# Kernel tuning notes

Hardware: AMD Instinct MI355X
Metric: run time of the kernel (lower is better)

The kernel has to match this reference:

```python
import jax, jax.numpy as jnp
import numpy as np

N, D, F, O = 32768, 32, 128, 128  # nodes, fixed in-degree, in_feats, out_feats


def _lstm_reduce(m, W_ih, W_hh, b_ih, b_hh):
    """Run an LSTM over each node's neighbor mailbox m: [N, T, F] -> final h: [N, H].
    PyTorch gate order: i, f, g, o. W_ih: [4H, F], W_hh: [4H, H]."""
    n, _, _ = m.shape
    H = W_hh.shape[1]
    b = b_ih + b_hh

    def step(carry, x_t):
        h, c = carry
        gates = x_t @ W_ih.T + h @ W_hh.T + b  # [N, 4H]
        i, f, g, o = jnp.split(gates, 4, axis=-1)
        c = jax.nn.sigmoid(f) * c + jax.nn.sigmoid(i) * jnp.tanh(g)
        h = jax.nn.sigmoid(o) * jnp.tanh(c)
        return (h, c), None

    h0 = jnp.zeros((n, H), m.dtype)
    (h_final, _), _ = jax.lax.scan(step, (h0, h0), jnp.swapaxes(m, 0, 1))
    return h_final


def setup_inputs() -> dict:
    key = jax.random.key(0)
    ks = jax.random.split(key, 9)
    stdv_lin = 1.0 / np.sqrt(F)   # linear init: uniform(-1/sqrt(in_feats))
    stdv_lstm = 1.0 / np.sqrt(F)  # torch LSTM init: uniform(-1/sqrt(hidden))
    u = lambda k, shape, s: jax.random.uniform(k, shape, jnp.float32, -s, s)
    return {
        "feat": jax.random.normal(ks[0], (N, F), jnp.float32),
        "neigh_idx": jax.random.randint(ks[1], (N, D), 0, N, jnp.int32),
        "W_ih": u(ks[2], (4 * F, F), stdv_lstm),
        "W_hh": u(ks[3], (4 * F, F), stdv_lstm),
        "b_ih": u(ks[4], (4 * F,), stdv_lstm),
        "b_hh": u(ks[5], (4 * F,), stdv_lstm),
        "W1": u(ks[6], (O, F), stdv_lin),
        "b1": u(ks[6], (O,), stdv_lin),
        "W2": u(ks[7], (O, F), stdv_lin),
        "b2": u(ks[8], (O,), stdv_lin),
    }


def reference(feat, neigh_idx, W_ih, W_hh, b_ih, b_hh, W1, b1, W2, b2):
    # Mailbox gather: each node's D neighbor feature rows -> [N, D, F]
    m = feat[neigh_idx]
    # LSTM reducer -> final hidden state per node
    h = _lstm_reduce(m, W_ih, W_hh, b_ih, b_hh)  # [N, F]
    degs = jnp.asarray(neigh_idx.shape[1], feat.dtype)  # fixed-degree graph
    ah = h / degs
    # feat = linear1(feat) + linear2(ah)
    return feat @ W1.T + b1 + ah @ W2.T + b2
```

## Files before the change

kernel.cpp:

```cpp
#include <hip/hip_runtime.h>
#include <hip/hip_bf16.h>

#define NN 32768
#define DEG 32
#define FF 128
#define OO 128
#define MB 32
#define MB2 16

#define K1 1.4426950408889634f
#define K2 2.8853900817779268f

#define PPITCH 1040
#define P0OFF 0
#define P1OFF 16640
#define H0OFF 33280
#define H1OFF 37376
#define LDSSZ 41472

typedef __attribute__((ext_vector_type(8))) short bfrag;
typedef __attribute__((ext_vector_type(4))) float f32x4;

__device__ __forceinline__ unsigned short b16(float x) {
    unsigned u = __float_as_uint(x) + 0x8000u;
    return (unsigned short)(u >> 16);
}
__device__ __forceinline__ float bf2f(unsigned short u) {
    return __uint_as_float((unsigned)u << 16);
}
__device__ __forceinline__ bfrag pack8(float4 a, float4 b) {
    bfrag r;
    r[0] = (short)b16(a.x); r[1] = (short)b16(a.y); r[2] = (short)b16(a.z); r[3] = (short)b16(a.w);
    r[4] = (short)b16(b.x); r[5] = (short)b16(b.y); r[6] = (short)b16(b.z); r[7] = (short)b16(b.w);
    return r;
}
__device__ __forceinline__ void gload16(const void* g, void* l) {
    __builtin_amdgcn_global_load_lds(
        (const __attribute__((address_space(1))) unsigned int*)g,
        (__attribute__((address_space(3))) unsigned int*)l, 16, 0, 0);
}

__global__ void prep_weights(const float* __restrict__ wih, const float* __restrict__ whh,
                             const float* __restrict__ b_ih, const float* __restrict__ b_hh,
                             const float* __restrict__ w1, const float* __restrict__ b1,
                             const float* __restrict__ w2, const float* __restrict__ b2,
                             short* __restrict__ wihb, short* __restrict__ whhb,
                             short* __restrict__ w1b, short* __restrict__ w2b,
                             float* __restrict__ biasg, float* __restrict__ biaso)
{
    int i = blockIdx.x * blockDim.x + threadIdx.x;
    if (i < 512 * 128) { wihb[i] = (short)b16(wih[i]); whhb[i] = (short)b16(whh[i]); }
    if (i < 128 * 128) { w1b[i] = (short)b16(w1[i]); w2b[i] = (short)b16(w2[i] * 0.03125f); }
    if (i < 512) biasg[i] = b_ih[i] + b_hh[i];
    if (i < 128) biaso[i] = b1[i] + b2[i];
}

__global__ __launch_bounds__(512, 2)
void xp_gemm(const float* __restrict__ feat, const short* __restrict__ wihb,
             const float* __restrict__ biasg, unsigned short* __restrict__ xp)
{
    __shared__ short xt[MB * 128];

    const int tid  = (int)threadIdx.x;
    const int lane = tid & 63;
    const int wave = tid >> 6;
    const int n0   = (int)blockIdx.x * MB;
    const int srow = tid >> 4;
    const int cs   = tid & 15;

    {   const float4* p = reinterpret_cast<const float4*>(feat + (n0 + srow) * FF + cs * 8);
        int sb = (srow * 256 + cs * 16) ^ ((srow & 7) << 4);
        *reinterpret_cast<bfrag*>(reinterpret_cast<char*>(xt) + sb) = pack8(p[0], p[1]); }

    const int colw = wave * 16 + (lane & 15);
    bfrag wih[4][4];
#pragma unroll
    for (int g = 0; g < 4; ++g) {
        const short* pih = wihb + (g * 128 + colw) * FF + (lane >> 4) * 8;
#pragma unroll
        for (int kt = 0; kt < 4; ++kt)
            wih[g][kt] = *reinterpret_cast<const bfrag*>(pih + kt * 32);
    }
    float bg4[4];
#pragma unroll
    for (int g = 0; g < 4; ++g) bg4[g] = biasg[g * 128 + colw];

    __syncthreads();

    const int arow = lane & 15;
    const int asub = (lane >> 4) * 16;
    const int hr0  = (lane >> 4) * 4;
    const int swz  = (arow & 7) << 4;
    const char* xtp = reinterpret_cast<const char*>(xt);

#pragma unroll
    for (int rt = 0; rt < 2; ++rt) {
        bfrag a[4];
#pragma unroll
        for (int kt = 0; kt < 4; ++kt)
            a[kt] = *reinterpret_cast<const bfrag*>(xtp + (((rt * 16 + arow) * 256 + kt * 64 + asub) ^ swz));
#pragma unroll
        for (int g = 0; g < 4; ++g) {
            f32x4 acc = {bg4[g], bg4[g], bg4[g], bg4[g]};
#pragma unroll
            for (int kt = 0; kt < 4; ++kt)
                acc = __builtin_amdgcn_mfma_f32_16x16x32_bf16(a[kt], wih[g][kt], acc, 0, 0, 0);
#pragma unroll
            for (int r = 0; r < 4; ++r)
                xp[(n0 + rt * 16 + hr0 + r) * 512 + g * 128 + colw] = b16(acc[r]);
        }
    }
}

__global__ __launch_bounds__(256, 2)
void sage_xp2(const float* __restrict__ feat, const int* __restrict__ nidx,
              const unsigned short* __restrict__ xp,
              const short* __restrict__ whhb, const short* __restrict__ w1b,
              const short* __restrict__ w2b, const float* __restrict__ biaso,
              float* __restrict__ out)
{
    __shared__ char lds[LDSSZ];
    __shared__ int  idx_s[MB2 * DEG];

    const int tid  = (int)threadIdx.x;
    const int lane = tid & 63;
    const int wave = tid >> 6;
    const int n0   = (int)blockIdx.x * MB2;
    const int srow = tid >> 4;
    const int cs   = tid & 15;

    idx_s[tid]       = nidx[n0 * DEG + tid];
    idx_s[256 + tid] = nidx[n0 * DEG + 256 + tid];
    {   bfrag z = {0, 0, 0, 0, 0, 0, 0, 0};
        *reinterpret_cast<bfrag*>(lds + H0OFF + tid * 16) = z; }

    const int colb = wave * 32 + (lane & 15);
    bfrag whh[2][4][4];
#pragma unroll
    for (int ct = 0; ct < 2; ++ct)
#pragma unroll
        for (int g = 0; g < 4; ++g) {
            const short* phh = whhb + (g * 128 + colb + ct * 16) * FF + (lane >> 4) * 8;
#pragma unroll
            for (int kt = 0; kt < 4; ++kt)
                whh[ct][g][kt] = *reinterpret_cast<const bfrag*>(phh + kt * 32);
        }
    __syncthreads();

#pragma unroll
    for (int j = 0; j < 4; ++j) {
        int nd = idx_s[(wave * 4 + j) * DEG + 0];
        gload16(xp + nd * 512 + lane * 8, lds + P0OFF + (wave * 4 + j) * PPITCH);
    }
    __syncthreads();

    const int arow = lane & 15;
    const int asub = (lane >> 4) * 16;
    const int hr0  = (lane >> 4) * 4;
    const int swz  = (arow & 7) << 4;

    f32x4 cs0 = {0.f, 0.f, 0.f, 0.f};
    f32x4 cs1 = {0.f, 0.f, 0.f, 0.f};

    auto rdP = [&](const char* pc, int goff) {
        f32x4 v;
        v[0] = bf2f(*reinterpret_cast<const unsigned short*>(pc + goff));
        v[1] = bf2f(*reinterpret_cast<const unsigned short*>(pc + goff + PPITCH));
        v[2] = bf2f(*reinterpret_cast<const unsigned short*>(pc + goff + 2 * PPITCH));
        v[3] = bf2f(*reinterpret_cast<const unsigned short*>(pc + goff + 3 * PPITCH));
        return v;
    };

    auto doct = [&](int ct, const bfrag (&ha)[4], int pcur, int hnxt, f32x4& cst) {
        const int colw = colb + ct * 16;
        const char* pc = lds + pcur + hr0 * PPITCH + colw * 2;
        f32x4 gi = rdP(pc, 0), gf = rdP(pc, 256), gg = rdP(pc, 512), go = rdP(pc, 768);
#pragma unroll
        for (int kt = 0; kt < 4; ++kt) {
            gi = __builtin_amdgcn_mfma_f32_16x16x32_bf16(ha[kt], whh[ct][0][kt], gi, 0, 0, 0);
            gf = __builtin_amdgcn_mfma_f32_16x16x32_bf16(ha[kt], whh[ct][1][kt], gf, 0, 0, 0);
            gg = __builtin_amdgcn_mfma_f32_16x16x32_bf16(ha[kt], whh[ct][2][kt], gg, 0, 0, 0);
            go = __builtin_amdgcn_mfma_f32_16x16x32_bf16(ha[kt], whh[ct][3][kt], go, 0, 0, 0);
        }
#pragma unroll
        for (int r = 0; r < 4; ++r) {
            float av = __builtin_amdgcn_exp2f(-K1 * gi[r]);
            float bv = __builtin_amdgcn_exp2f(K2 * fminf(gg[r], 40.0f));
            float dv = __builtin_amdgcn_exp2f(-K1 * gf[r]);
            float ev = __builtin_amdgcn_exp2f(-K1 * go[r]);
            float t1 = __builtin_amdgcn_rcpf((1.0f + av) * (1.0f + bv));
            float t2 = __builtin_amdgcn_rcpf(1.0f + dv);
            float c  = fmaf(cst[r], t2, (bv - 1.0f) * t1);
            cst[r] = c;
            float uv = __builtin_amdgcn_exp2f(K2 * c);
            float t3 = __builtin_amdgcn_rcpf((1.0f + ev) * (1.0f + uv));
            float h  = (uv - 1.0f) * t3;
            int hrow = hr0 + r;
            int hb   = (hrow * 256 + colw * 2) ^ ((hrow & 7) << 4);
            *reinterpret_cast<unsigned short*>(lds + hnxt + hb) = b16(h);
        }
    };

#define STEP(T, PCUR, PNXT, HCUR, HNXT)                                         \
    {                                                                           \
        if ((T) < DEG - 1) {                                                    \
            _Pragma("unroll")                                                   \
            for (int j = 0; j < 4; ++j) {                                       \
                int nd = idx_s[(wave * 4 + j) * DEG + (T) + 1];                 \
                gload16(xp + nd * 512 + lane * 8,                               \
                        lds + (PNXT) + (wave * 4 + j) * PPITCH);                \
            }                                                                   \
        }                                                                       \
        bfrag ha[4];                                                            \
        _Pragma("unroll")                                                       \
        for (int kt = 0; kt < 4; ++kt)                                          \
            ha[kt] = *reinterpret_cast<const bfrag*>(                           \
                lds + (HCUR) + ((arow * 256 + kt * 64 + asub) ^ swz));          \
        doct(0, ha, PCUR, HNXT, cs0);                                           \
        doct(1, ha, PCUR, HNXT, cs1);                                           \
        __syncthreads();                                                        \
    }

#pragma unroll 1
    for (int tt = 0; tt < DEG; tt += 2) {
        STEP(tt,     P0OFF, P1OFF, H0OFF, H1OFF);
        STEP(tt + 1, P1OFF, P0OFF, H1OFF, H0OFF);
    }
#undef STEP

    {   const float4* p = reinterpret_cast<const float4*>(feat + (n0 + srow) * FF + cs * 8);
        int sb = (srow * 256 + cs * 16) ^ ((srow & 7) << 4);
        *reinterpret_cast<bfrag*>(lds + P0OFF + sb) = pack8(p[0], p[1]); }
    __syncthreads();

    bfrag w1f[2][4], w2f[2][4];
    float bb[2];
#pragma unroll
    for (int ct = 0; ct < 2; ++ct) {
        const int colw = colb + ct * 16;
#pragma unroll
        for (int kt = 0; kt < 4; ++kt) {
            w1f[ct][kt] = *reinterpret_cast<const bfrag*>(w1b + colw * FF + kt * 32 + (lane >> 4) * 8);
            w2f[ct][kt] = *reinterpret_cast<const bfrag*>(w2b + colw * FF + kt * 32 + (lane >> 4) * 8);
        }
        bb[ct] = biaso[colw];
    }
    bfrag fa[4], hfa[4];
#pragma unroll
    for (int kt = 0; kt < 4; ++kt) {
        int byte = (arow * 256 + kt * 64 + asub) ^ swz;
        fa[kt]  = *reinterpret_cast<const bfrag*>(lds + P0OFF + byte);
        hfa[kt] = *reinterpret_cast<const bfrag*>(lds + H0OFF + byte);
    }
#pragma unroll
    for (int ct = 0; ct < 2; ++ct) {
        f32x4 acc = {0.f, 0.f, 0.f, 0.f};
#pragma unroll
        for (int kt = 0; kt < 4; ++kt) {
            acc = __builtin_amdgcn_mfma_f32_16x16x32_bf16(fa[kt],  w1f[ct][kt], acc, 0, 0, 0);
            acc = __builtin_amdgcn_mfma_f32_16x16x32_bf16(hfa[kt], w2f[ct][kt], acc, 0, 0, 0);
        }
#pragma unroll
        for (int r = 0; r < 4; ++r) {
            int orow = n0 + hr0 + r;
            out[orow * OO + colb + ct * 16] = acc[r] + bb[ct];
        }
    }
}

__global__ __launch_bounds__(512, 2)
void sage_lstm_fb(const float* __restrict__ featf, const int* __restrict__ nidx,
                  const short* __restrict__ wihb, const short* __restrict__ whhb,
                  const short* __restrict__ w1b, const short* __restrict__ w2b,
                  const float* __restrict__ biasg, const float* __restrict__ biaso,
                  float* __restrict__ out)
{
    __shared__ short xbuf[2][MB * 128];
    __shared__ short hbuf[2][MB * 128];
    __shared__ int   idx_s[MB * DEG];

    const int tid  = (int)threadIdx.x;
    const int lane = tid & 63;
    const int wave = tid >> 6;
    const int n0   = (int)blockIdx.x * MB;
    const int srow = tid >> 4;
    const int cs   = tid & 15;

    idx_s[tid]       = nidx[n0 * DEG + tid];
    idx_s[512 + tid] = nidx[n0 * DEG + 512 + tid];
    {   bfrag z = {0, 0, 0, 0, 0, 0, 0, 0};
        reinterpret_cast<bfrag*>(hbuf[0])[tid] = z; }

    const int colw = wave * 16 + (lane & 15);
    bfrag wih[4][4], whh[4][4];
#pragma unroll
    for (int g = 0; g < 4; ++g) {
        const short* pih = wihb + (g * 128 + colw) * FF + (lane >> 4) * 8;
        const short* phh = whhb + (g * 128 + colw) * FF + (lane >> 4) * 8;
#pragma unroll
        for (int kt = 0; kt < 4; ++kt) {
            wih[g][kt] = *reinterpret_cast<const bfrag*>(pih + kt * 32);
            whh[g][kt] = *reinterpret_cast<const bfrag*>(phh + kt * 32);
        }
    }
    const float bi = biasg[colw];
    const float bf = biasg[128 + colw];
    const float bg = biasg[256 + colw];
    const float bo = biasg[384 + colw];
    const f32x4 bvi = {bi, bi, bi, bi};
    const f32x4 bvf = {bf, bf, bf, bf};
    const f32x4 bvg = {bg, bg, bg, bg};
    const f32x4 bvo = {bo, bo, bo, bo};

    __syncthreads();
    {
        const float4* p = reinterpret_cast<const float4*>(featf + idx_s[srow * DEG] * FF + cs * 8);
        int sb = (srow * 256 + cs * 16) ^ ((srow & 7) << 4);
        *reinterpret_cast<bfrag*>(reinterpret_cast<char*>(xbuf[0]) + sb) = pack8(p[0], p[1]);
    }
    __syncthreads();

    const int arow = lane & 15;
    const int asub = (lane >> 4) * 16;
    const int hr0  = (lane >> 4) * 4;
    const int swz  = (arow & 7) << 4;

    auto mm4 = [&](const char* p, int rbase, const bfrag (&W)[4][4],
                   f32x4& vi, f32x4& vf, f32x4& vg, f32x4& vo) {
        bfrag a[4];
#pragma unroll
        for (int kt = 0; kt < 4; ++kt)
            a[kt] = *reinterpret_cast<const bfrag*>(p + ((rbase * 256 + kt * 64 + asub) ^ swz));
#pragma unroll
        for (int kt = 0; kt < 4; ++kt) {
            vi = __builtin_amdgcn_mfma_f32_16x16x32_bf16(a[kt], W[0][kt], vi, 0, 0, 0);
            vf = __builtin_amdgcn_mfma_f32_16x16x32_bf16(a[kt], W[1][kt], vf, 0, 0, 0);
            vg = __builtin_amdgcn_mfma_f32_16x16x32_bf16(a[kt], W[2][kt], vg, 0, 0, 0);
            vo = __builtin_amdgcn_mfma_f32_16x16x32_bf16(a[kt], W[3][kt], vo, 0, 0, 0);
        }
    };
    auto actw = [&](f32x4& gi, f32x4& gf, f32x4& gg, f32x4& go,
                    f32x4& cst, char* hnxt, int rt) {
#pragma unroll
        for (int r = 0; r < 4; ++r) {
            float av = __builtin_amdgcn_exp2f(-K1 * gi[r]);
            float bv = __builtin_amdgcn_exp2f(K2 * fminf(gg[r], 40.0f));
            float dv = __builtin_amdgcn_exp2f(-K1 * gf[r]);
            float ev = __builtin_amdgcn_exp2f(-K1 * go[r]);
            float t1 = __builtin_amdgcn_rcpf((1.0f + av) * (1.0f + bv));
            float t2 = __builtin_amdgcn_rcpf(1.0f + dv);
            float c  = fmaf(cst[r], t2, (bv - 1.0f) * t1);
            cst[r] = c;
            float uv = __builtin_amdgcn_exp2f(K2 * c);
            float t3 = __builtin_amdgcn_rcpf((1.0f + ev) * (1.0f + uv));
            float h  = (uv - 1.0f) * t3;
            int hrow = rt * 16 + hr0 + r;
            int hb   = (hrow * 256 + colw * 2) ^ ((hrow & 7) << 4);
            *reinterpret_cast<unsigned short*>(hnxt + hb) = b16(h);
        }
    };

    f32x4 p0i, p0f, p0g, p0o, p1i, p1f, p1g, p1o;
    {
        char* x0p = reinterpret_cast<char*>(xbuf[0]);
        p0i = bvi; p0f = bvf; p0g = bvg; p0o = bvo;
        mm4(x0p, arow, wih, p0i, p0f, p0g, p0o);
        p1i = bvi; p1f = bvf; p1g = bvg; p1o = bvo;
        mm4(x0p, 16 + arow, wih, p1i, p1f, p1g, p1o);
    }
    {
        const float4* p = reinterpret_cast<const float4*>(featf + idx_s[srow * DEG + 1] * FF + cs * 8);
        int sb = (srow * 256 + cs * 16) ^ ((srow & 7) << 4);
        *reinterpret_cast<bfrag*>(reinterpret_cast<char*>(xbuf[1]) + sb) = pack8(p[0], p[1]);
    }
    __syncthreads();

    const f32x4 zz = {0.f, 0.f, 0.f, 0.f};
    f32x4 cs0 = zz, cs1 = zz;

#pragma unroll 2
    for (int t = 0; t < DEG; ++t) {
        const int cur = t & 1;
        char* hcur = reinterpret_cast<char*>(hbuf[cur]);
        char* hnxt = reinterpret_cast<char*>(hbuf[cur ^ 1]);
        char* xrd  = reinterpret_cast<char*>(xbuf[cur ^ 1]);
        char* xwr  = reinterpret_cast<char*>(xbuf[cur]);

        bfrag pre2;
        if (t < DEG - 2) {
            const float4* p = reinterpret_cast<const float4*>(featf + idx_s[srow * DEG + t + 2] * FF + cs * 8);
            pre2 = pack8(p[0], p[1]);
        }
        {
            f32x4 gi = p0i, gf = p0f, gg = p0g, go = p0o;
            mm4(hcur, arow, whh, gi, gf, gg, go);
            if (t < DEG - 1) {
                p0i = bvi; p0f = bvf; p0g = bvg; p0o = bvo;
                mm4(xrd, arow, wih, p0i, p0f, p0g, p0o);
            }
            actw(gi, gf, gg, go, cs0, hnxt, 0);
        }
        {
            f32x4 gi = p1i, gf = p1f, gg = p1g, go = p1o;
            mm4(hcur, 16 + arow, whh, gi, gf, gg, go);
            if (t < DEG - 1) {
                p1i = bvi; p1f = bvf; p1g = bvg; p1o = bvo;
                mm4(xrd, 16 + arow, wih, p1i, p1f, p1g, p1o);
            }
            actw(gi, gf, gg, go, cs1, hnxt, 1);
        }
        if (t < DEG - 2) {
            int sb = (srow * 256 + cs * 16) ^ ((srow & 7) << 4);
            *reinterpret_cast<bfrag*>(xwr + sb) = pre2;
        }
        __syncthreads();
    }

    {
        const float4* p = reinterpret_cast<const float4*>(featf + (n0 + srow) * FF + cs * 8);
        int sb = (srow * 256 + cs * 16) ^ ((srow & 7) << 4);
        *reinterpret_cast<bfrag*>(reinterpret_cast<char*>(xbuf[0]) + sb) = pack8(p[0], p[1]);
    }
    __syncthreads();

    char* const x0p = reinterpret_cast<char*>(xbuf[0]);
    char* const h0p = reinterpret_cast<char*>(hbuf[0]);
    bfrag w1f[4], w2f[4];
#pragma unroll
    for (int kt = 0; kt < 4; ++kt) {
        w1f[kt] = *reinterpret_cast<const bfrag*>(w1b + colw * FF + kt * 32 + (lane >> 4) * 8);
        w2f[kt] = *reinterpret_cast<const bfrag*>(w2b + colw * FF + kt * 32 + (lane >> 4) * 8);
    }
    const float bb = biaso[colw];
#pragma unroll
    for (int rt = 0; rt < 2; ++rt) {
        bfrag fa[4], hfa[4];
#pragma unroll
        for (int kt = 0; kt < 4; ++kt) {
            int byte = ((rt * 16 + arow) * 256 + kt * 64 + asub) ^ swz;
            fa[kt]  = *reinterpret_cast<const bfrag*>(x0p + byte);
            hfa[kt] = *reinterpret_cast<const bfrag*>(h0p + byte);
        }
        f32x4 acc = {0.f, 0.f, 0.f, 0.f};
#pragma unroll
        for (int kt = 0; kt < 4; ++kt) {
            acc = __builtin_amdgcn_mfma_f32_16x16x32_bf16(fa[kt],  w1f[kt], acc, 0, 0, 0);
            acc = __builtin_amdgcn_mfma_f32_16x16x32_bf16(hfa[kt], w2f[kt], acc, 0, 0, 0);
        }
#pragma unroll
        for (int r = 0; r < 4; ++r) {
            int orow = n0 + rt * 16 + hr0 + r;
            out[orow * OO + colw] = acc[r] + bb;
        }
    }
}

extern "C" void kernel_launch(void* const* d_in, const int* in_sizes, int n_in,
                              void* d_out, int out_size, void* d_ws, size_t ws_size,
                              hipStream_t stream)
{
    const float* feat = (const float*)d_in[0];
    const int*   nidx = (const int*)d_in[1];
    const float* W_ih = (const float*)d_in[2];
    const float* W_hh = (const float*)d_in[3];
    const float* b_ih = (const float*)d_in[4];
    const float* b_hh = (const float*)d_in[5];
    const float* W1   = (const float*)d_in[6];
    const float* b1   = (const float*)d_in[7];
    const float* W2   = (const float*)d_in[8];
    const float* b2   = (const float*)d_in[9];
    float* out = (float*)d_out;

    char* ws = (char*)d_ws;
    short* wihb  = (short*)(ws);
    short* whhb  = (short*)(ws + 131072);
    short* w1b   = (short*)(ws + 262144);
    short* w2b   = (short*)(ws + 294912);
    float* biasg = (float*)(ws + 327680);
    float* biaso = (float*)(ws + 329728);
    unsigned short* xpb = (unsigned short*)(ws + 330240);

    const size_t need = 330240 + (size_t)NN * 512 * 2;

    prep_weights<<<256, 256, 0, stream>>>(W_ih, W_hh, b_ih, b_hh, W1, b1, W2, b2,
                                          wihb, whhb, w1b, w2b, biasg, biaso);
    if (ws_size >= need) {
        xp_gemm<<<NN / MB, 512, 0, stream>>>(feat, wihb, biasg, xpb);
        sage_xp2<<<NN / MB2, 256, 0, stream>>>(feat, nidx, xpb, whhb, w1b, w2b, biaso, out);
    } else {
        sage_lstm_fb<<<NN / MB, 512, 0, stream>>>(feat, nidx, wihb, whhb,
                                                  w1b, w2b, biasg, biaso, out);
    }
}
```

Before: 307.5 us.

## Triple-buffer neighbor xp prefetch and interleave gate layout for vector LDS reads

The recurrent LSTM kernel now prefetches projected neighbor rows two timesteps ahead using three LDS buffers. It waits with a partial vmcnt instead of a full sync, so global gathers overlap more compute. The xp projection is stored gate-interleaved (i,f,g,o per column), letting each thread read all four gate pre-activations with one 8-byte LDS load instead of four scalar loads. The cost is more LDS per block, which may limit occupancy, plus hand-written waitcnt and barrier logic that is fragile if the instruction count assumptions break.

```diff
diff --git a/kernel.cpp b/kernel.cpp
--- a/kernel.cpp
+++ b/kernel.cpp
@@ -14,9 +14,10 @@
 #define PPITCH 1040
 #define P0OFF 0
 #define P1OFF 16640
-#define H0OFF 33280
-#define H1OFF 37376
-#define LDSSZ 41472
+#define P2OFF 33280
+#define H0OFF 49920
+#define H1OFF 54016
+#define LDSSZ 58112
 
 typedef __attribute__((ext_vector_type(8))) short bfrag;
 typedef __attribute__((ext_vector_type(4))) float f32x4;
@@ -99,21 +100,29 @@
 #pragma unroll
         for (int kt = 0; kt < 4; ++kt)
             a[kt] = *reinterpret_cast<const bfrag*>(xtp + (((rt * 16 + arow) * 256 + kt * 64 + asub) ^ swz));
-#pragma unroll
-        for (int g = 0; g < 4; ++g) {
-            f32x4 acc = {bg4[g], bg4[g], bg4[g], bg4[g]};
-#pragma unroll
-            for (int kt = 0; kt < 4; ++kt)
-                acc = __builtin_amdgcn_mfma_f32_16x16x32_bf16(a[kt], wih[g][kt], acc, 0, 0, 0);
-#pragma unroll
-            for (int r = 0; r < 4; ++r)
-                xp[(n0 + rt * 16 + hr0 + r) * 512 + g * 128 + colw] = b16(acc[r]);
+        f32x4 acc0 = {bg4[0], bg4[0], bg4[0], bg4[0]};
+        f32x4 acc1 = {bg4[1], bg4[1], bg4[1], bg4[1]};
+        f32x4 acc2 = {bg4[2], bg4[2], bg4[2], bg4[2]};
+        f32x4 acc3 = {bg4[3], bg4[3], bg4[3], bg4[3]};
+#pragma unroll
+        for (int kt = 0; kt < 4; ++kt) {
+            acc0 = __builtin_amdgcn_mfma_f32_16x16x32_bf16(a[kt], wih[0][kt], acc0, 0, 0, 0);
+            acc1 = __builtin_amdgcn_mfma_f32_16x16x32_bf16(a[kt], wih[1][kt], acc1, 0, 0, 0);
+            acc2 = __builtin_amdgcn_mfma_f32_16x16x32_bf16(a[kt], wih[2][kt], acc2, 0, 0, 0);
+            acc3 = __builtin_amdgcn_mfma_f32_16x16x32_bf16(a[kt], wih[3][kt], acc3, 0, 0, 0);
+        }
+#pragma unroll
+        for (int r = 0; r < 4; ++r) {
+            ushort4 pk;
+            pk.x = b16(acc0[r]); pk.y = b16(acc1[r]);
+            pk.z = b16(acc2[r]); pk.w = b16(acc3[r]);
+            *reinterpret_cast<ushort4*>(xp + (size_t)(n0 + rt * 16 + hr0 + r) * 512 + colw * 4) = pk;
         }
     }
 }
 
 __global__ __launch_bounds__(256, 2)
-void sage_xp2(const float* __restrict__ feat, const int* __restrict__ nidx,
+void sage_xp3(const float* __restrict__ feat, const int* __restrict__ nidx,
               const unsigned short* __restrict__ xp,
               const short* __restrict__ whhb, const short* __restrict__ w1b,
               const short* __restrict__ w2b, const float* __restrict__ biaso,
@@ -149,10 +158,18 @@
 
 #pragma unroll
     for (int j = 0; j < 4; ++j) {
-        int nd = idx_s[(wave * 4 + j) * DEG + 0];
-        gload16(xp + nd * 512 + lane * 8, lds + P0OFF + (wave * 4 + j) * PPITCH);
-    }
-    __syncthreads();
+        int nd0 = idx_s[(wave * 4 + j) * DEG + 0];
+        gload16(xp + (size_t)nd0 * 512 + lane * 8, lds + P0OFF + (wave * 4 + j) * PPITCH);
+    }
+#pragma unroll
+    for (int j = 0; j < 4; ++j) {
+        int nd1 = idx_s[(wave * 4 + j) * DEG + 1];
+        gload16(xp + (size_t)nd1 * 512 + lane * 8, lds + P1OFF + (wave * 4 + j) * PPITCH);
+    }
+    asm volatile("s_waitcnt vmcnt(4)" ::: "memory");
+    __builtin_amdgcn_sched_barrier(0);
+    __builtin_amdgcn_s_barrier();
+    __builtin_amdgcn_sched_barrier(0);
 
     const int arow = lane & 15;
     const int asub = (lane >> 4) * 16;
@@ -162,19 +179,15 @@
     f32x4 cs0 = {0.f, 0.f, 0.f, 0.f};
     f32x4 cs1 = {0.f, 0.f, 0.f, 0.f};
 
-    auto rdP = [&](const char* pc, int goff) {
-        f32x4 v;
-        v[0] = bf2f(*reinterpret_cast<const unsigned short*>(pc + goff));
-        v[1] = bf2f(*reinterpret_cast<const unsigned short*>(pc + goff + PPITCH));
-        v[2] = bf2f(*reinterpret_cast<const unsigned short*>(pc + goff + 2 * PPITCH));
-        v[3] = bf2f(*reinterpret_cast<const unsigned short*>(pc + goff + 3 * PPITCH));
-        return v;
-    };
-
     auto doct = [&](int ct, const bfrag (&ha)[4], int pcur, int hnxt, f32x4& cst) {
         const int colw = colb + ct * 16;
-        const char* pc = lds + pcur + hr0 * PPITCH + colw * 2;
-        f32x4 gi = rdP(pc, 0), gf = rdP(pc, 256), gg = rdP(pc, 512), go = rdP(pc, 768);
+        const char* pc = lds + pcur + hr0 * PPITCH + colw * 8;
+        f32x4 gi, gf, gg, go;
+#pragma unroll
+        for (int r = 0; r < 4; ++r) {
+            ushort4 pv = *reinterpret_cast<const ushort4*>(pc + r * PPITCH);
+            gi[r] = bf2f(pv.x); gf[r] = bf2f(pv.y); gg[r] = bf2f(pv.z); go[r] = bf2f(pv.w);
+        }
 #pragma unroll
         for (int kt = 0; kt < 4; ++kt) {
             gi = __builtin_amdgcn_mfma_f32_16x16x32_bf16(ha[kt], whh[ct][0][kt], gi, 0, 0, 0);
@@ -201,15 +214,13 @@
         }
     };
 
-#define STEP(T, PCUR, PNXT, HCUR, HNXT)                                         \
+#define STEPC(T, PCUR, PNXT, HCUR, HNXT)                                        \
     {                                                                           \
-        if ((T) < DEG - 1) {                                                    \
-            _Pragma("unroll")                                                   \
-            for (int j = 0; j < 4; ++j) {                                       \
-                int nd = idx_s[(wave * 4 + j) * DEG + (T) + 1];                 \
-                gload16(xp + nd * 512 + lane * 8,                               \
-                        lds + (PNXT) + (wave * 4 + j) * PPITCH);                \
-            }                                                                   \
+        _Pragma("unroll")                                                       \
+        for (int j = 0; j < 4; ++j) {                                           \
+            int nd = idx_s[(wave * 4 + j) * DEG + (T) + 2];                     \
+            gload16(xp + (size_t)nd * 512 + lane * 8,                           \
+                    lds + (PNXT) + (wave * 4 + j) * PPITCH);                    \
         }                                                                       \
         bfrag ha[4];                                                            \
         _Pragma("unroll")                                                       \
@@ -218,15 +229,38 @@
                 lds + (HCUR) + ((arow * 256 + kt * 64 + asub) ^ swz));          \
         doct(0, ha, PCUR, HNXT, cs0);                                           \
         doct(1, ha, PCUR, HNXT, cs1);                                           \
+        asm volatile("s_waitcnt lgkmcnt(0)" ::: "memory");                      \
+        asm volatile("s_waitcnt vmcnt(4)" ::: "memory");                        \
+        __builtin_amdgcn_sched_barrier(0);                                      \
+        __builtin_amdgcn_s_barrier();                                           \
+        __builtin_amdgcn_sched_barrier(0);                                      \
+    }
+
+#define STEPF(T, PCUR, HCUR, HNXT)                                              \
+    {                                                                           \
+        bfrag ha[4];                                                            \
+        _Pragma("unroll")                                                       \
+        for (int kt = 0; kt < 4; ++kt)                                          \
+            ha[kt] = *reinterpret_cast<const bfrag*>(                           \
+                lds + (HCUR) + ((arow * 256 + kt * 64 + asub) ^ swz));          \
+        doct(0, ha, PCUR, HNXT, cs0);                                           \
+        doct(1, ha, PCUR, HNXT, cs1);                                           \
         __syncthreads();                                                        \
     }
 
 #pragma unroll 1
-    for (int tt = 0; tt < DEG; tt += 2) {
-        STEP(tt,     P0OFF, P1OFF, H0OFF, H1OFF);
-        STEP(tt + 1, P1OFF, P0OFF, H1OFF, H0OFF);
-    }
-#undef STEP
+    for (int b6 = 0; b6 < 30; b6 += 6) {
+        STEPC(b6 + 0, P0OFF, P2OFF, H0OFF, H1OFF);
+        STEPC(b6 + 1, P1OFF, P0OFF, H1OFF, H0OFF);
+        STEPC(b6 + 2, P2OFF, P1OFF, H0OFF, H1OFF);
+        STEPC(b6 + 3, P0OFF, P2OFF, H1OFF, H0OFF);
+        STEPC(b6 + 4, P1OFF, P0OFF, H0OFF, H1OFF);
+        STEPC(b6 + 5, P2OFF, P1OFF, H1OFF, H0OFF);
+    }
+    STEPF(30, P0OFF, H0OFF, H1OFF);
+    STEPF(31, P1OFF, H1OFF, H0OFF);
+#undef STEPC
+#undef STEPF
 
     {   const float4* p = reinterpret_cast<const float4*>(feat + (n0 + srow) * FF + cs * 8);
         int sb = (srow * 256 + cs * 16) ^ ((srow & 7) << 4);
@@ -486,7 +520,7 @@
                                           wihb, whhb, w1b, w2b, biasg, biaso);
     if (ws_size >= need) {
         xp_gemm<<<NN / MB, 512, 0, stream>>>(feat, wihb, biasg, xpb);
-        sage_xp2<<<NN / MB2, 256, 0, stream>>>(feat, nidx, xpb, whhb, w1b, w2b, biaso, out);
+        sage_xp3<<<NN / MB2, 256, 0, stream>>>(feat, nidx, xpb, whhb, w1b, w2b, biaso, out);
     } else {
         sage_lstm_fb<<<NN / MB, 512, 0, stream>>>(feat, nidx, wihb, whhb,
                                                   w1b, w2b, biasg, biaso, out);
```

Result: faster. 300.0 us (-2.4%).
